# Kernel optimization log

Measured on AMD Instinct MI355X. Metric: run time of the kernel, lower is better.

The kernel has to match this reference:

```python
import jax, jax.numpy as jnp
import numpy as np

N_HEADS = 16
ROPE_BASE = 10000.0


def _rope_tables(T, head_dim, dtype):
    d2 = head_dim // 2
    inv_freq = 1.0 / (ROPE_BASE ** (jnp.arange(0, head_dim, 2, dtype=jnp.float32) / head_dim))
    t = jnp.arange(T, dtype=jnp.float32)
    freqs = jnp.outer(t, inv_freq)  # [T, d2]
    cos = jnp.cos(freqs)[None, :, None, :].astype(dtype)  # [1,T,1,d2]
    sin = jnp.sin(freqs)[None, :, None, :].astype(dtype)
    return cos, sin


def _apply_rotary(x, cos, sin):
    # x: [B,T,H,D]; rotate halves
    d = x.shape[-1] // 2
    x1, x2 = x[..., :d], x[..., d:]
    return jnp.concatenate([x1 * cos + x2 * sin, -x1 * sin + x2 * cos], axis=-1)


def setup_inputs() -> dict:
    key = jax.random.key(0)
    k1, k2, k3 = jax.random.split(key, 3)
    B, T, C = 2, 2048, 1024
    x = jax.random.normal(k1, (B, T, C), dtype=jnp.float32)
    w_attn = jax.random.normal(k2, (3 * C, C), dtype=jnp.float32) * (1.0 / np.sqrt(C))
    w_proj = jax.random.normal(k3, (C, C), dtype=jnp.float32) * (1.0 / np.sqrt(C))
    return {"x": x, "w_attn": w_attn, "w_proj": w_proj}


def reference(x, w_attn, w_proj):
    B, T, C = x.shape
    H = N_HEADS
    D = C // H
    qkv = jnp.einsum('btc,fc->btf', x, w_attn)  # [B,T,3C]
    q, k, v = jnp.split(qkv, 3, axis=2)
    q = q.reshape(B, T, H, D)
    k = k.reshape(B, T, H, D)
    v = v.reshape(B, T, H, D)
    cos, sin = _rope_tables(T, D, x.dtype)
    q = _apply_rotary(q, cos, sin)
    k = _apply_rotary(k, cos, sin)
    # causal SDPA, scale 1/sqrt(D)
    scale = 1.0 / np.sqrt(D)
    scores = jnp.einsum('bqhd,bkhd->bhqk', q, k) * scale
    causal = jnp.tril(jnp.ones((T, T), dtype=bool))
    scores = jnp.where(causal[None, None], scores, jnp.finfo(scores.dtype).min)
    attn = jax.nn.softmax(scores, axis=-1)
    y = jnp.einsum('bhqk,bkhd->bqhd', attn, v).reshape(B, T, C)
    return jnp.einsum('btc,oc->bto', y, w_proj)
```

## Files before the change

kernel.cpp:

```cpp
#include <hip/hip_runtime.h>
#include <math.h>

typedef __bf16 bf16x8 __attribute__((ext_vector_type(8)));
typedef float f32x4 __attribute__((ext_vector_type(4)));

__device__ __forceinline__ unsigned f2bf(float f) {
    union { float f; unsigned u; } v; v.f = f;
    return (v.u + 0x7FFFu + ((v.u >> 16) & 1u)) >> 16;
}

__device__ __forceinline__ unsigned cvtpk(float a, float b) {
    unsigned r;
    __asm__("v_cvt_pk_bf16_f32 %0, %1, %2" : "=v"(r) : "v"(a), "v"(b));
    return r;
}

__device__ __forceinline__ void gload16(const ushort* g, ushort* l) {
    __builtin_amdgcn_global_load_lds(
        (const __attribute__((address_space(1))) void*)g,
        (__attribute__((address_space(3))) void*)l, 16, 0, 0);
}

__device__ __forceinline__ bool src_is_fp32(const unsigned* s) {
    int sane = 0;
#pragma unroll
    for (int i = 0; i < 64; ++i) {
        unsigned lo = s[i] & 0xFFFFu;
        unsigned e = (lo >> 7) & 0xFF;
        if (lo == 0u || (e >= 100u && e <= 140u)) sane++;
    }
    return sane < 48;
}

__global__ __launch_bounds__(256) void tobf16_all_kernel(
    const unsigned* __restrict__ s0, const unsigned* __restrict__ s1,
    const unsigned* __restrict__ s2,
    ushort* __restrict__ d0, ushort* __restrict__ d1, ushort* __restrict__ d2) {
    const int bx = blockIdx.x;
    const unsigned* src;
    ushort* dst;
    int lb;
    if (bx < 2048)      { src = s0; dst = d0; lb = bx; }
    else if (bx < 3584) { src = s1; dst = d1; lb = bx - 2048; }
    else                { src = s2; dst = d2; lb = bx - 3584; }
    const int i = lb * 2048 + threadIdx.x * 8;
    if (src_is_fp32(src)) {
        const float* fs = (const float*)src;
        float4 f0 = *(const float4*)(fs + i);
        float4 f1 = *(const float4*)(fs + i + 4);
        uint4 o;
        o.x = f2bf(f0.x) | (f2bf(f0.y) << 16);
        o.y = f2bf(f0.z) | (f2bf(f0.w) << 16);
        o.z = f2bf(f1.x) | (f2bf(f1.y) << 16);
        o.w = f2bf(f1.z) | (f2bf(f1.w) << 16);
        *(uint4*)(dst + i) = o;
    } else {
        *(uint4*)(dst + i) = *(const uint4*)((const ushort*)src + i);
    }
}

constexpr int GBM = 128, GBN = 128, GBK = 32;

__global__ __launch_bounds__(256) void gemm_qkv_rope_kernel(
    const ushort* __restrict__ A, const ushort* __restrict__ Bmat,
    ushort* __restrict__ qkvh, int K) {
    __shared__ ushort As[2][GBM * GBK];
    __shared__ ushort Bs[2][GBN * GBK];

    const int tid  = threadIdx.x;
    const int lane = tid & 63;
    const int wv   = tid >> 6;
    const int wm   = (wv >> 1) * 64;
    const int wn   = (wv & 1) * 64;

    const ushort* Ab = A + (size_t)blockIdx.x * GBM * K;
    const ushort* Bb = Bmat + (size_t)blockIdx.y * GBN * K;

    f32x4 acc[4][4];
#pragma unroll
    for (int i = 0; i < 4; i++)
#pragma unroll
        for (int j = 0; j < 4; j++) acc[i][j] = (f32x4){0.f, 0.f, 0.f, 0.f};

    const int srow = tid >> 2;
    const int scol = (tid & 3) * 8;
    const int fr = lane & 15;
    const int fk = (lane >> 4) * 8;
    const int nK = K >> 5;

    gload16(Ab + (size_t)srow * K + scol,        As[0] + wv * 512);
    gload16(Ab + (size_t)(srow + 64) * K + scol, As[0] + wv * 512 + 2048);
    gload16(Bb + (size_t)srow * K + scol,        Bs[0] + wv * 512);
    gload16(Bb + (size_t)(srow + 64) * K + scol, Bs[0] + wv * 512 + 2048);

#pragma unroll 1
    for (int it = 0; it < nK; ++it) {
        const int cur = it & 1;
        __syncthreads();
        if (it + 1 < nK) {
            const int k0 = (it + 1) << 5, nxt = cur ^ 1;
            gload16(Ab + (size_t)srow * K + k0 + scol,        As[nxt] + wv * 512);
            gload16(Ab + (size_t)(srow + 64) * K + k0 + scol, As[nxt] + wv * 512 + 2048);
            gload16(Bb + (size_t)srow * K + k0 + scol,        Bs[nxt] + wv * 512);
            gload16(Bb + (size_t)(srow + 64) * K + k0 + scol, Bs[nxt] + wv * 512 + 2048);
        }
        bf16x8 af[4], bfr[4];
#pragma unroll
        for (int i = 0; i < 4; i++)
            af[i] = *(const bf16x8*)(As[cur] + (wm + i * 16 + fr) * GBK + fk);
#pragma unroll
        for (int j = 0; j < 4; j++)
            bfr[j] = *(const bf16x8*)(Bs[cur] + (wn + j * 16 + fr) * GBK + fk);
#pragma unroll
        for (int i = 0; i < 4; i++)
#pragma unroll
            for (int j = 0; j < 4; j++)
                acc[i][j] = __builtin_amdgcn_mfma_f32_16x16x32_bf16(af[i], bfr[j], acc[i][j], 0, 0, 0);
    }

    const int crow0 = (lane >> 4) * 4;
    const int col0  = blockIdx.y * GBN + wn;
    const int which = col0 >> 10;
    const int hh    = (col0 >> 6) & 15;
    ushort* outp = qkvh + (size_t)which * 4194304 + (size_t)hh * 131072;

    if (which < 2) {
        const float inva = exp2f((float)fr * -0.41524101186f);
        const float invb = exp2f((float)(fr + 16) * -0.41524101186f);
        const float qs = (which == 0) ? 0.125f : 1.0f;
#pragma unroll
        for (int i = 0; i < 4; i++)
#pragma unroll
            for (int r = 0; r < 4; r++) {
                int row = blockIdx.x * GBM + wm + i * 16 + crow0 + r;
                int t = row & 2047;
                size_t ob = ((size_t)(row >> 11)) * 2097152 + (size_t)t * 64;
                float sa, ca, sb, cb;
                __sincosf((float)t * inva, &sa, &ca);
                __sincosf((float)t * invb, &sb, &cb);
                float q0 = acc[i][0][r], q1 = acc[i][1][r];
                float q2 = acc[i][2][r], q3 = acc[i][3][r];
                float n0 = (q0 * ca + q2 * sa) * qs;
                float n1 = (q1 * cb + q3 * sb) * qs;
                float n2 = (q2 * ca - q0 * sa) * qs;
                float n3 = (q3 * cb - q1 * sb) * qs;
                unsigned u01 = cvtpk(n0, n1);
                unsigned u23 = cvtpk(n2, n3);
                outp[ob + fr]      = (ushort)(u01 & 0xFFFFu);
                outp[ob + 16 + fr] = (ushort)(u01 >> 16);
                outp[ob + 32 + fr] = (ushort)(u23 & 0xFFFFu);
                outp[ob + 48 + fr] = (ushort)(u23 >> 16);
            }
    } else {
#pragma unroll
        for (int i = 0; i < 4; i++)
#pragma unroll
            for (int r = 0; r < 4; r++) {
                int row = blockIdx.x * GBM + wm + i * 16 + crow0 + r;
                int t = row & 2047;
                size_t ob = ((size_t)(row >> 11)) * 2097152 + (size_t)t * 64;
                unsigned u01 = cvtpk(acc[i][0][r], acc[i][1][r]);
                unsigned u23 = cvtpk(acc[i][2][r], acc[i][3][r]);
                outp[ob + fr]      = (ushort)(u01 & 0xFFFFu);
                outp[ob + 16 + fr] = (ushort)(u01 >> 16);
                outp[ob + 32 + fr] = (ushort)(u23 & 0xFFFFu);
                outp[ob + 48 + fr] = (ushort)(u23 >> 16);
            }
    }
}

__global__ __launch_bounds__(256) void gemm_bt_kernel(
    const ushort* __restrict__ A, const ushort* __restrict__ Bmat,
    float* __restrict__ C, int M, int N, int K) {
    __shared__ ushort As[2][GBM * GBK];
    __shared__ ushort Bs[2][GBN * GBK];

    const int tid  = threadIdx.x;
    const int lane = tid & 63;
    const int wv   = tid >> 6;
    const int wm   = (wv >> 1) * 64;
    const int wn   = (wv & 1) * 64;

    const ushort* Ab = A + (size_t)blockIdx.x * GBM * K;
    const ushort* Bb = Bmat + (size_t)blockIdx.y * GBN * K;

    f32x4 acc[4][4];
#pragma unroll
    for (int i = 0; i < 4; i++)
#pragma unroll
        for (int j = 0; j < 4; j++) acc[i][j] = (f32x4){0.f, 0.f, 0.f, 0.f};

    const int srow = tid >> 2;
    const int scol = (tid & 3) * 8;
    const int fr = lane & 15;
    const int fk = (lane >> 4) * 8;
    const int nK = K >> 5;

    gload16(Ab + (size_t)srow * K + scol,        As[0] + wv * 512);
    gload16(Ab + (size_t)(srow + 64) * K + scol, As[0] + wv * 512 + 2048);
    gload16(Bb + (size_t)srow * K + scol,        Bs[0] + wv * 512);
    gload16(Bb + (size_t)(srow + 64) * K + scol, Bs[0] + wv * 512 + 2048);

#pragma unroll 1
    for (int it = 0; it < nK; ++it) {
        const int cur = it & 1;
        __syncthreads();
        if (it + 1 < nK) {
            const int k0 = (it + 1) << 5, nxt = cur ^ 1;
            gload16(Ab + (size_t)srow * K + k0 + scol,        As[nxt] + wv * 512);
            gload16(Ab + (size_t)(srow + 64) * K + k0 + scol, As[nxt] + wv * 512 + 2048);
            gload16(Bb + (size_t)srow * K + k0 + scol,        Bs[nxt] + wv * 512);
            gload16(Bb + (size_t)(srow + 64) * K + k0 + scol, Bs[nxt] + wv * 512 + 2048);
        }
        bf16x8 af[4], bfr[4];
#pragma unroll
        for (int i = 0; i < 4; i++)
            af[i] = *(const bf16x8*)(As[cur] + (wm + i * 16 + fr) * GBK + fk);
#pragma unroll
        for (int j = 0; j < 4; j++)
            bfr[j] = *(const bf16x8*)(Bs[cur] + (wn + j * 16 + fr) * GBK + fk);
#pragma unroll
        for (int i = 0; i < 4; i++)
#pragma unroll
            for (int j = 0; j < 4; j++)
                acc[i][j] = __builtin_amdgcn_mfma_f32_16x16x32_bf16(af[i], bfr[j], acc[i][j], 0, 0, 0);
    }

    const int crow0 = (lane >> 4) * 4;
#pragma unroll
    for (int i = 0; i < 4; i++)
#pragma unroll
        for (int j = 0; j < 4; j++)
#pragma unroll
            for (int r = 0; r < 4; r++) {
                int row = blockIdx.x * GBM + wm + i * 16 + crow0 + r;
                int col = blockIdx.y * GBN + wn + j * 16 + fr;
                C[(size_t)row * N + col] = acc[i][j][r];
            }
}

#define NEG_BIG (-1e30f)
constexpr int LPK = 72;
constexpr int LPV = 136;

__global__ __launch_bounds__(1024) void attn_kernel(const ushort* __restrict__ qkvh,
                                                    ushort* __restrict__ y) {
    __shared__ ushort Ks[2][128 * LPK];
    __shared__ ushort Vt[2][64 * LPV];

    const int tid  = threadIdx.x;
    const int lane = tid & 63;
    const int wv   = tid >> 6;
    const int half = wv >> 3;
    const int wq   = wv & 7;
    const int jb   = half * 4;
    const int pid  = blockIdx.x;
    const int bh   = blockIdx.y;
    const int b    = bh >> 4, h = bh & 15;

    const ushort* qp = qkvh + (size_t)b * 2097152 + (size_t)h * 131072;
    const ushort* kp = qp + 4194304;
    const ushort* vp = qp + 8388608;

    const int fr = lane & 15;
    const int fq = lane >> 4;
    const int fk = fq * 8;

    const int srow = tid >> 3;
    const int scol = (tid & 7) * 8;
    const int vkey = tid & 127;
    const int vd0  = (tid >> 7) * 8;

    const int slA = fr + 32 * (fq & 1);
    const int slB = slA + 16;
    const bool hi = (fq >> 1) != 0;

#pragma unroll 1
    for (int seg = 0; seg < 2; ++seg) {
        const int qb = seg ? (15 - pid) : pid;
        const int nIt = qb + 1;

        __syncthreads();

        const int qrow = qb * 128 + wq * 16 + fr;
        bf16x8 qf0 = *(const bf16x8*)(qp + (size_t)qrow * 64 + fk);
        bf16x8 qf1 = *(const bf16x8*)(qp + (size_t)qrow * 64 + 32 + fk);

        f32x4 o[4];
        o[0] = o[1] = o[2] = o[3] = (f32x4){0.f, 0.f, 0.f, 0.f};
        float lsum = 0.f;

        uint4 kr, vr;
        {
            kr = *(const uint4*)(kp + (size_t)srow * 64 + scol);
            vr = *(const uint4*)(vp + (size_t)vkey * 64 + vd0);
            *(uint4*)(Ks[0] + srow * LPK + scol) = kr;
            unsigned w[4] = {vr.x, vr.y, vr.z, vr.w};
#pragma unroll
            for (int t = 0; t < 4; ++t) {
                Vt[0][(vd0 + 2 * t)     * LPV + vkey] = (ushort)(w[t] & 0xFFFFu);
                Vt[0][(vd0 + 2 * t + 1) * LPV + vkey] = (ushort)(w[t] >> 16);
            }
        }
        if (1 < nIt) {
            kr = *(const uint4*)(kp + (size_t)(128 + srow) * 64 + scol);
            vr = *(const uint4*)(vp + (size_t)(128 + vkey) * 64 + vd0);
        }

#pragma unroll 1
        for (int it = 0; it < nIt; ++it) {
            const int cur = it & 1;
            const int k0 = it * 128;
            __syncthreads();
            if (it + 1 < nIt) {
                const int nxt = cur ^ 1;
                *(uint4*)(Ks[nxt] + srow * LPK + scol) = kr;
                unsigned w[4] = {vr.x, vr.y, vr.z, vr.w};
#pragma unroll
                for (int t = 0; t < 4; ++t) {
                    Vt[nxt][(vd0 + 2 * t)     * LPV + vkey] = (ushort)(w[t] & 0xFFFFu);
                    Vt[nxt][(vd0 + 2 * t + 1) * LPV + vkey] = (ushort)(w[t] >> 16);
                }
                if (it + 2 < nIt) {
                    kr = *(const uint4*)(kp + (size_t)(k0 + 256 + srow) * 64 + scol);
                    vr = *(const uint4*)(vp + (size_t)(k0 + 256 + vkey) * 64 + vd0);
                }
            }

            f32x4 s[4];
#pragma unroll
            for (int jl = 0; jl < 4; ++jl) {
                const int j = jb + jl;
                bf16x8 kf0 = *(const bf16x8*)(Ks[cur] + (j * 16 + fr) * LPK + fk);
                bf16x8 kf1 = *(const bf16x8*)(Ks[cur] + (j * 16 + fr) * LPK + 32 + fk);
                f32x4 z = (f32x4){0.f, 0.f, 0.f, 0.f};
                z = __builtin_amdgcn_mfma_f32_16x16x32_bf16(kf0, qf0, z, 0, 0, 0);
                z = __builtin_amdgcn_mfma_f32_16x16x32_bf16(kf1, qf1, z, 0, 0, 0);
                s[jl] = z;
            }
            if (it + 1 < nIt) {
#pragma unroll
                for (int jl = 0; jl < 4; ++jl)
#pragma unroll
                    for (int r = 0; r < 4; ++r) {
                        float p = __expf(s[jl][r]);
                        s[jl][r] = p;
                        lsum += p;
                    }
            } else {
#pragma unroll
                for (int jl = 0; jl < 4; ++jl)
#pragma unroll
                    for (int r = 0; r < 4; ++r) {
                        float v = s[jl][r];
                        if ((k0 + (jb + jl) * 16 + fq * 4 + r) > qrow) v = NEG_BIG;
                        float p = __expf(v);
                        s[jl][r] = p;
                        lsum += p;
                    }
            }

            unsigned u0[4], u1[4];
#pragma unroll
            for (int jl = 0; jl < 4; ++jl) {
                u0[jl] = cvtpk(s[jl][0], s[jl][1]);
                u1[jl] = cvtpk(s[jl][2], s[jl][3]);
            }
            unsigned A0[4], A1[4], B0[4], B1[4];
#pragma unroll
            for (int jl = 0; jl < 4; ++jl) {
                A0[jl] = __shfl(u0[jl], slA, 64);
                A1[jl] = __shfl(u1[jl], slA, 64);
                B0[jl] = __shfl(u0[jl], slB, 64);
                B1[jl] = __shfl(u1[jl], slB, 64);
            }

#pragma unroll
            for (int kl = 0; kl < 2; ++kl) {
                union { unsigned u[4]; bf16x8 v; } pa;
                pa.u[0] = hi ? A0[2 * kl + 1] : A0[2 * kl];
                pa.u[1] = hi ? A1[2 * kl + 1] : A1[2 * kl];
                pa.u[2] = hi ? B0[2 * kl + 1] : B0[2 * kl];
                pa.u[3] = hi ? B1[2 * kl + 1] : B1[2 * kl];
                const int vcol = half * 64 + kl * 32 + fk;
#pragma unroll
                for (int j4 = 0; j4 < 4; ++j4) {
                    bf16x8 vf = *(const bf16x8*)(Vt[cur] + (j4 * 16 + fr) * LPV + vcol);
                    o[j4] = __builtin_amdgcn_mfma_f32_16x16x32_bf16(pa.v, vf, o[j4], 0, 0, 0);
                }
            }
        }

        lsum += __shfl_xor(lsum, 16, 64);
        lsum += __shfl_xor(lsum, 32, 64);

        __syncthreads();
        float* ex = (float*)(&Ks[0][0]) + wq * 1104;
        if (half) {
#pragma unroll
            for (int j4 = 0; j4 < 4; ++j4)
#pragma unroll
                for (int r = 0; r < 4; ++r)
                    ex[lane * 17 + j4 * 4 + r] = o[j4][r];
            if (fq == 0) ex[1088 + fr] = lsum;
        }
        __syncthreads();
        if (!half) {
            float linv[4];
#pragma unroll
            for (int r = 0; r < 4; ++r) {
                float own = __shfl(lsum, fq * 4 + r, 64);
                linv[r] = 1.0f / (own + ex[1088 + fq * 4 + r]);
            }
#pragma unroll
            for (int j4 = 0; j4 < 4; j4 += 2)
#pragma unroll
                for (int r = 0; r < 4; ++r) {
                    int row = qb * 128 + wq * 16 + fq * 4 + r;
                    size_t yb = ((size_t)b * 2048 + row) * 1024 + h * 64;
                    float v0 = (o[j4][r]     + ex[lane * 17 + j4 * 4 + r])       * linv[r];
                    float v1 = (o[j4 + 1][r] + ex[lane * 17 + (j4 + 1) * 4 + r]) * linv[r];
                    unsigned u = cvtpk(v0, v1);
                    y[yb + j4 * 16 + fr]       = (ushort)(u & 0xFFFFu);
                    y[yb + (j4 + 1) * 16 + fr] = (ushort)(u >> 16);
                }
        }
    }
}

extern "C" void kernel_launch(void* const* d_in, const int* in_sizes, int n_in,
                              void* d_out, int out_size, void* d_ws, size_t ws_size,
                              hipStream_t stream) {
    const int nx = in_sizes[0];
    const int na = in_sizes[1];
    const int np = in_sizes[2];

    ushort* qkvh = (ushort*)d_ws;
    ushort* yb   = qkvh + (size_t)3 * 4194304;
    ushort* xb   = yb + (size_t)4096 * 1024;
    ushort* wab  = xb + nx;
    ushort* wpb  = wab + na;
    size_t need = ((size_t)3 * 4194304 + (size_t)4096 * 1024 + nx + na + np) * 2;
    if (ws_size < need) return;

    tobf16_all_kernel<<<dim3(4096), 256, 0, stream>>>(
        (const unsigned*)d_in[0], (const unsigned*)d_in[1], (const unsigned*)d_in[2],
        xb, wab, wpb);

    gemm_qkv_rope_kernel<<<dim3(32, 24), 256, 0, stream>>>(xb, wab, qkvh, 1024);
    attn_kernel<<<dim3(8, 32), 1024, 0, stream>>>(qkvh, yb);
    gemm_bt_kernel<<<dim3(32, 8), 256, 0, stream>>>(yb, wpb, (float*)d_out, 4096, 1024, 1024);
}
```

Baseline: 190.5 us.

## Load K tiles directly to swizzled LDS and transpose P through LDS

K tiles are now copied straight from global memory into LDS with global_load_lds. They land in an XOR-swizzled, unpadded layout, so K no longer passes through registers, and the K-fragment reads use matching swizzled offsets. The softmax probabilities are handed to the P·V MFMA through a per-wave LDS scratch buffer, replacing the cross-lane shuffle and select sequence. This cuts register traffic and VALU/shuffle work but adds LDS round-trips and raises LDS use to about 104 KB per block. It also relies on async-to-LDS loads being correctly waited on before the barriers.

```diff
diff --git a/kernel.cpp b/kernel.cpp
--- a/kernel.cpp
+++ b/kernel.cpp
@@ -240,13 +240,14 @@
 }
 
 #define NEG_BIG (-1e30f)
-constexpr int LPK = 72;
-constexpr int LPV = 136;
+constexpr int VT_OFF = 16384;
+constexpr int LPV    = 136;
+constexpr int PS_OFF = VT_OFF + 2 * 64 * LPV;
+constexpr int LPP    = 72;
 
 __global__ __launch_bounds__(1024) void attn_kernel(const ushort* __restrict__ qkvh,
                                                     ushort* __restrict__ y) {
-    __shared__ ushort Ks[2][128 * LPK];
-    __shared__ ushort Vt[2][64 * LPV];
+    __shared__ ushort SM[PS_OFF + 16 * 16 * LPP];
 
     const int tid  = threadIdx.x;
     const int lane = tid & 63;
@@ -266,14 +267,15 @@
     const int fq = lane >> 4;
     const int fk = fq * 8;
 
-    const int srow = tid >> 3;
-    const int scol = (tid & 7) * 8;
+    const int krow = tid >> 3;
+    const int kblk = tid & 7;
+    const int ksrc = krow * 64 + ((kblk ^ (krow & 7)) << 3);
+    const int koff0 = (fq ^ (fr & 7)) << 3;
+    const int koff1 = koff0 ^ 32;
     const int vkey = tid & 127;
     const int vd0  = (tid >> 7) * 8;
 
-    const int slA = fr + 32 * (fq & 1);
-    const int slB = slA + 16;
-    const bool hi = (fq >> 1) != 0;
+    ushort* pw = SM + PS_OFF + wv * (16 * LPP);
 
 #pragma unroll 1
     for (int seg = 0; seg < 2; ++seg) {
@@ -282,6 +284,20 @@
 
         __syncthreads();
 
+        gload16(kp + ksrc, SM + wv * 512);
+        uint4 vr = *(const uint4*)(vp + (size_t)vkey * 64 + vd0);
+        {
+            unsigned w[4] = {vr.x, vr.y, vr.z, vr.w};
+            ushort* vt0 = SM + VT_OFF;
+#pragma unroll
+            for (int t = 0; t < 4; ++t) {
+                vt0[(vd0 + 2 * t)     * LPV + vkey] = (ushort)(w[t] & 0xFFFFu);
+                vt0[(vd0 + 2 * t + 1) * LPV + vkey] = (ushort)(w[t] >> 16);
+            }
+        }
+        if (1 < nIt)
+            vr = *(const uint4*)(vp + (size_t)(128 + vkey) * 64 + vd0);
+
         const int qrow = qb * 128 + wq * 16 + fr;
         bf16x8 qf0 = *(const bf16x8*)(qp + (size_t)qrow * 64 + fk);
         bf16x8 qf1 = *(const bf16x8*)(qp + (size_t)qrow * 64 + 32 + fk);
@@ -289,50 +305,34 @@
         f32x4 o[4];
         o[0] = o[1] = o[2] = o[3] = (f32x4){0.f, 0.f, 0.f, 0.f};
         float lsum = 0.f;
-
-        uint4 kr, vr;
-        {
-            kr = *(const uint4*)(kp + (size_t)srow * 64 + scol);
-            vr = *(const uint4*)(vp + (size_t)vkey * 64 + vd0);
-            *(uint4*)(Ks[0] + srow * LPK + scol) = kr;
-            unsigned w[4] = {vr.x, vr.y, vr.z, vr.w};
-#pragma unroll
-            for (int t = 0; t < 4; ++t) {
-                Vt[0][(vd0 + 2 * t)     * LPV + vkey] = (ushort)(w[t] & 0xFFFFu);
-                Vt[0][(vd0 + 2 * t + 1) * LPV + vkey] = (ushort)(w[t] >> 16);
-            }
-        }
-        if (1 < nIt) {
-            kr = *(const uint4*)(kp + (size_t)(128 + srow) * 64 + scol);
-            vr = *(const uint4*)(vp + (size_t)(128 + vkey) * 64 + vd0);
-        }
 
 #pragma unroll 1
         for (int it = 0; it < nIt; ++it) {
             const int cur = it & 1;
             const int k0 = it * 128;
+            const ushort* Ksc = SM + cur * 8192;
+            const ushort* Vtc = SM + VT_OFF + cur * (64 * LPV);
             __syncthreads();
             if (it + 1 < nIt) {
                 const int nxt = cur ^ 1;
-                *(uint4*)(Ks[nxt] + srow * LPK + scol) = kr;
+                gload16(kp + (it + 1) * 8192 + ksrc, SM + nxt * 8192 + wv * 512);
+                ushort* vtn = SM + VT_OFF + nxt * (64 * LPV);
                 unsigned w[4] = {vr.x, vr.y, vr.z, vr.w};
 #pragma unroll
                 for (int t = 0; t < 4; ++t) {
-                    Vt[nxt][(vd0 + 2 * t)     * LPV + vkey] = (ushort)(w[t] & 0xFFFFu);
-                    Vt[nxt][(vd0 + 2 * t + 1) * LPV + vkey] = (ushort)(w[t] >> 16);
+                    vtn[(vd0 + 2 * t)     * LPV + vkey] = (ushort)(w[t] & 0xFFFFu);
+                    vtn[(vd0 + 2 * t + 1) * LPV + vkey] = (ushort)(w[t] >> 16);
                 }
-                if (it + 2 < nIt) {
-                    kr = *(const uint4*)(kp + (size_t)(k0 + 256 + srow) * 64 + scol);
+                if (it + 2 < nIt)
                     vr = *(const uint4*)(vp + (size_t)(k0 + 256 + vkey) * 64 + vd0);
-                }
             }
 
             f32x4 s[4];
 #pragma unroll
             for (int jl = 0; jl < 4; ++jl) {
-                const int j = jb + jl;
-                bf16x8 kf0 = *(const bf16x8*)(Ks[cur] + (j * 16 + fr) * LPK + fk);
-                bf16x8 kf1 = *(const bf16x8*)(Ks[cur] + (j * 16 + fr) * LPK + 32 + fk);
+                const int row = ((jb + jl) * 16 + fr) * 64;
+                bf16x8 kf0 = *(const bf16x8*)(Ksc + row + koff0);
+                bf16x8 kf1 = *(const bf16x8*)(Ksc + row + koff1);
                 f32x4 z = (f32x4){0.f, 0.f, 0.f, 0.f};
                 z = __builtin_amdgcn_mfma_f32_16x16x32_bf16(kf0, qf0, z, 0, 0, 0);
                 z = __builtin_amdgcn_mfma_f32_16x16x32_bf16(kf1, qf1, z, 0, 0, 0);
@@ -360,33 +360,23 @@
                     }
             }
 
-            unsigned u0[4], u1[4];
 #pragma unroll
             for (int jl = 0; jl < 4; ++jl) {
-                u0[jl] = cvtpk(s[jl][0], s[jl][1]);
-                u1[jl] = cvtpk(s[jl][2], s[jl][3]);
-            }
-            unsigned A0[4], A1[4], B0[4], B1[4];
-#pragma unroll
-            for (int jl = 0; jl < 4; ++jl) {
-                A0[jl] = __shfl(u0[jl], slA, 64);
-                A1[jl] = __shfl(u1[jl], slA, 64);
-                B0[jl] = __shfl(u0[jl], slB, 64);
-                B1[jl] = __shfl(u1[jl], slB, 64);
-            }
+                uint2 u;
+                u.x = cvtpk(s[jl][0], s[jl][1]);
+                u.y = cvtpk(s[jl][2], s[jl][3]);
+                *(uint2*)(pw + fr * LPP + jl * 16 + fq * 4) = u;
+            }
+            __asm__ volatile("" ::: "memory");
 
 #pragma unroll
             for (int kl = 0; kl < 2; ++kl) {
-                union { unsigned u[4]; bf16x8 v; } pa;
-                pa.u[0] = hi ? A0[2 * kl + 1] : A0[2 * kl];
-                pa.u[1] = hi ? A1[2 * kl + 1] : A1[2 * kl];
-                pa.u[2] = hi ? B0[2 * kl + 1] : B0[2 * kl];
-                pa.u[3] = hi ? B1[2 * kl + 1] : B1[2 * kl];
+                bf16x8 pf = *(const bf16x8*)(pw + fr * LPP + kl * 32 + fk);
                 const int vcol = half * 64 + kl * 32 + fk;
 #pragma unroll
                 for (int j4 = 0; j4 < 4; ++j4) {
-                    bf16x8 vf = *(const bf16x8*)(Vt[cur] + (j4 * 16 + fr) * LPV + vcol);
-                    o[j4] = __builtin_amdgcn_mfma_f32_16x16x32_bf16(pa.v, vf, o[j4], 0, 0, 0);
+                    bf16x8 vf = *(const bf16x8*)(Vtc + (j4 * 16 + fr) * LPV + vcol);
+                    o[j4] = __builtin_amdgcn_mfma_f32_16x16x32_bf16(pf, vf, o[j4], 0, 0, 0);
                 }
             }
         }
@@ -395,7 +385,7 @@
         lsum += __shfl_xor(lsum, 32, 64);
 
         __syncthreads();
-        float* ex = (float*)(&Ks[0][0]) + wq * 1104;
+        float* ex = (float*)(SM + PS_OFF) + wq * 1104;
         if (half) {
 #pragma unroll
             for (int j4 = 0; j4 < 4; ++j4)
```

New measurement: 189.2 us. No clear change (-0.7%).
